# Performance work log

Hardware: AMD Instinct MI355X
Metric: run time of the kernel (lower is better)

Reference implementation:

```python
import jax, jax.numpy as jnp
import numpy as np

WS = (7, 7)  # window size
NUM_HEADS = 16


def _relative_position_index(ws):
    # Deterministic int index table, computed exactly as in the torch module.
    coords = np.stack(np.meshgrid(np.arange(ws[0]), np.arange(ws[1]), indexing='ij'))  # [2,Wh,Ww]
    coords = coords.reshape(2, -1)                       # [2, N]
    rel = coords[:, :, None] - coords[:, None, :]        # [2, N, N]
    rel = rel.transpose(1, 2, 0)                         # [N, N, 2]
    rel = rel + np.array([ws[0] - 1, ws[1] - 1])
    rel[:, :, 0] *= 2 * ws[1] - 1
    return jnp.asarray(rel.sum(-1), dtype=jnp.int32)     # [N, N]


def setup_inputs() -> dict:
    key = jax.random.key(0)
    ks = jax.random.split(key, 5)
    B_, N, C = 2048, WS[0] * WS[1], 512
    nw = 64
    return {
        'x': jax.random.normal(ks[0], (B_, N, C), dtype=jnp.float32),
        'mask': jax.random.normal(ks[1], (nw, N, N), dtype=jnp.float32),
        'qkv_w': jax.random.normal(ks[2], (3 * C, C), dtype=jnp.float32) * 0.02,
        'qkv_b': jax.random.normal(ks[3], (3 * C,), dtype=jnp.float32) * 0.02,
        'rpb_table': jax.random.normal(ks[4], ((2 * WS[0] - 1) * (2 * WS[1] - 1), NUM_HEADS), dtype=jnp.float32) * 0.02,
    }


def reference(x, mask, qkv_w, qkv_b, rpb_table):
    B_, N, C = x.shape
    H = NUM_HEADS
    hd = C // H
    scale = hd ** -0.5

    # qkv projection: [B_, N, 3, H, hd] -> q, k, v each [B_, H, N, hd]
    qkv = (jnp.einsum('bnc,oc->bno', x, qkv_w) + qkv_b)
    qkv = qkv.reshape(B_, N, 3, H, hd).transpose(2, 0, 3, 1, 4)
    q, k, v = qkv[0], qkv[1], qkv[2]

    attn = jnp.einsum('bhnd,bhmd->bhnm', q * scale, k)  # [B_, H, N, N]

    rel_idx = _relative_position_index(WS)                       # [N, N]
    bias = rpb_table[rel_idx.reshape(-1)].reshape(N, N, H)       # gather
    attn = attn + bias.transpose(2, 0, 1)[None]                  # [1, H, N, N]

    nw = mask.shape[0]
    attn = attn.reshape(B_ // nw, nw, H, N, N) + mask[None, :, None]
    attn = attn.reshape(B_, H, N, N)
    attn = jax.nn.softmax(attn, axis=-1)

    out = jnp.einsum('bhnm,bhmd->bhnd', attn, v)
    out = out.transpose(0, 2, 1, 3).reshape(B_, N, C)
    # NOTE: source assigns `X = self.proj(x)` but returns `x`, so the
    # output projection is dead code; we faithfully return pre-proj output.
    return out
```

## Files before the change

kernel.cpp:

```cpp
#include <hip/hip_runtime.h>
#include <cstdint>
#include <cstddef>

typedef __bf16 bf16x8 __attribute__((ext_vector_type(8)));
typedef float f32x4 __attribute__((ext_vector_type(4)));
typedef unsigned short u16x8 __attribute__((ext_vector_type(8)));
typedef unsigned short u16x4 __attribute__((ext_vector_type(4)));
typedef unsigned int u32x2 __attribute__((ext_vector_type(2)));

#define VT_LD 56
#define BSTRIDE 52
#define BSZ 2548
#define PLD 80

__device__ __forceinline__ unsigned short f2bf(float f) {
  unsigned int u = __builtin_bit_cast(unsigned int, f);
  u += 0x7FFFu + ((u >> 16) & 1u);
  return (unsigned short)(u >> 16);
}
__device__ __forceinline__ float bf2f(unsigned short h) {
  unsigned int u = (unsigned int)h << 16;
  return __builtin_bit_cast(float, u);
}

__device__ __forceinline__ void gload_lds16(const void* g, void* l) {
  __builtin_amdgcn_global_load_lds((const __attribute__((address_space(1))) void*)g,
                                   (__attribute__((address_space(3))) void*)l, 16, 0, 0);
}

__global__ void conv_f2b_k(const float* __restrict__ src, unsigned short* __restrict__ dst, long n8) {
  long i = (long)blockIdx.x * blockDim.x + threadIdx.x;
  long stride = (long)gridDim.x * blockDim.x;
  for (; i < n8; i += stride) {
    float4 a = *(const float4*)(src + i * 8);
    float4 b = *(const float4*)(src + i * 8 + 4);
    u16x8 p;
    p[0]=f2bf(a.x); p[1]=f2bf(a.y); p[2]=f2bf(a.z); p[3]=f2bf(a.w);
    p[4]=f2bf(b.x); p[5]=f2bf(b.y); p[6]=f2bf(b.z); p[7]=f2bf(b.w);
    *(u16x8*)(dst + i * 8) = p;
  }
}

__global__ void build_bias_k(const float* __restrict__ rpb, unsigned short* __restrict__ biasT) {
  int idx = blockIdx.x * 256 + threadIdx.x;
  if (idx >= 16 * BSZ) return;
  int h = idx / BSZ;
  int rem = idx - h * BSZ;
  int i = rem / BSTRIDE, j = rem - (rem / BSTRIDE) * BSTRIDE;
  unsigned short v = 0;
  if (j < 49) {
    int r1 = i / 7, c1 = i - r1 * 7;
    int r2 = j / 7, c2 = j - r2 * 7;
    int ri = (r1 - r2 + 6) * 13 + (c1 - c2 + 6);
    v = f2bf(rpb[ri * 16 + h]);
  }
  biasT[idx] = v;
}

#define GEMM_SETUP(N0)                                                         \
  int t = threadIdx.x;                                                         \
  int lane = t & 63, wv = t >> 6;                                              \
  int g = lane >> 4, q = lane & 15;                                            \
  int wrow = wv >> 1, wcol = wv & 1;                                           \
  f32x4 acc[4][4] = {};                                                        \
  int schunk = (t & 3) ^ ((t >> 3) & 3);                                       \
  const unsigned short* ag0 = xb + (m0 + (t >> 2)) * 512 + schunk * 8;         \
  const unsigned short* ag1 = ag0 + 64 * 512;                                  \
  const unsigned short* bg0 = wb + (size_t)((N0) + (t >> 2)) * 512 + schunk * 8; \
  const unsigned short* bg1 = bg0 + 64 * 512;                                  \
  unsigned short* alA  = Ab + wv * 512;                                        \
  unsigned short* alA2 = Ab + 2048 + wv * 512;                                 \
  unsigned short* blB  = Bb + wv * 512;                                        \
  unsigned short* blB2 = Bb + 2048 + wv * 512;                                 \
  int roff = (8 * g) ^ (((q >> 1) & 3) << 3);                                  \
  const unsigned short* arb = Ab + (wrow * 64 + q) * 32 + roff;                \
  const unsigned short* brb = Bb + (wcol * 64 + q) * 32 + roff;

#define STAGE(KT, BOFF) do {                    \
    int kof = (KT) * 32;                        \
    gload_lds16(ag0 + kof, alA  + (BOFF));      \
    gload_lds16(ag1 + kof, alA2 + (BOFF));      \
    gload_lds16(bg0 + kof, blB  + (BOFF));      \
    gload_lds16(bg1 + kof, blB2 + (BOFF));      \
  } while (0)

#define COMPUTE(BOFF, SWAPPED) do {                                            \
    bf16x8 af[4], bfr[4];                                                      \
    _Pragma("unroll")                                                          \
    for (int i2 = 0; i2 < 4; ++i2) af[i2]  = *(const bf16x8*)(arb + (BOFF) + i2 * 512); \
    _Pragma("unroll")                                                          \
    for (int j2 = 0; j2 < 4; ++j2) bfr[j2] = *(const bf16x8*)(brb + (BOFF) + j2 * 512); \
    _Pragma("unroll")                                                          \
    for (int i2 = 0; i2 < 4; ++i2)                                             \
      _Pragma("unroll")                                                        \
      for (int j2 = 0; j2 < 4; ++j2)                                           \
        acc[i2][j2] = (SWAPPED)                                                \
          ? __builtin_amdgcn_mfma_f32_16x16x32_bf16(bfr[j2], af[i2], acc[i2][j2], 0, 0, 0) \
          : __builtin_amdgcn_mfma_f32_16x16x32_bf16(af[i2], bfr[j2], acc[i2][j2], 0, 0, 0); \
  } while (0)

#define KLOOP(SWAPPED)                          \
  STAGE(0, 0);                                  \
  __syncthreads();                              \
  for (int kt = 0; kt < 16; kt += 2) {          \
    STAGE(kt + 1, 4096);                        \
    COMPUTE(0, SWAPPED);                        \
    __syncthreads();                            \
    if (kt + 2 < 16) STAGE(kt + 2, 0);          \
    COMPUTE(4096, SWAPPED);                     \
    __syncthreads();                            \
  }

__global__ __launch_bounds__(256, 3) void qkv_gemm_k(
    const unsigned short* __restrict__ xb, const float* __restrict__ qkv_b,
    const unsigned short* __restrict__ wb,
    unsigned short* __restrict__ qs, unsigned short* __restrict__ kk,
    unsigned short* __restrict__ vt)
{
  __shared__ __align__(16) unsigned short smem[16384];
  unsigned short* Ab = smem;
  unsigned short* Bb = smem + 8192;

  int bid = blockIdx.x;
  int sw = (bid & 7) * 1176 + (bid >> 3);
  int mt = sw / 12, nt = sw - mt * 12;
  long m0 = (long)mt * 128;
  int  n0 = nt * 128;
  int  s  = n0 >> 9;

  GEMM_SETUP(n0)

  if (s < 2) {
    KLOOP(1)
    unsigned short* dst = (s == 0) ? qs : kk;
    float sc = (s == 0) ? 0.17677669529663687f : 1.0f;
    float4 bi[4];
    int hj[4], dj[4];
    #pragma unroll
    for (int j2 = 0; j2 < 4; ++j2) {
      int n = n0 + wcol * 64 + j2 * 16 + 4 * g;
      bi[j2] = *(const float4*)(qkv_b + n);
      hj[j2] = (n >> 5) & 15;
      dj[j2] = n & 31;
    }
    #pragma unroll
    for (int i2 = 0; i2 < 4; ++i2) {
      unsigned int m = (unsigned int)m0 + wrow * 64 + i2 * 16 + q;
      unsigned int b = m / 49;
      unsigned int i = m - b * 49;
      size_t base = ((size_t)(b * 16) * 49 + i) * 32;
      #pragma unroll
      for (int j2 = 0; j2 < 4; ++j2) {
        f32x4 a = acc[i2][j2];
        unsigned int lo = (unsigned int)f2bf((a[0] + bi[j2].x) * sc) | ((unsigned int)f2bf((a[1] + bi[j2].y) * sc) << 16);
        unsigned int hi = (unsigned int)f2bf((a[2] + bi[j2].z) * sc) | ((unsigned int)f2bf((a[3] + bi[j2].w) * sc) << 16);
        u32x2 wv2 = {lo, hi};
        *(u32x2*)(dst + base + (size_t)hj[j2] * (49 * 32) + dj[j2]) = wv2;
      }
    }
  } else {
    KLOOP(0)
    #pragma unroll
    for (int j2 = 0; j2 < 4; ++j2) {
      int n  = n0 + wcol * 64 + j2 * 16 + q;
      float bias = qkv_b[n];
      int d = n & 31;
      int h = (n >> 5) & 15;
      #pragma unroll
      for (int i2 = 0; i2 < 4; ++i2) {
        unsigned int gm0 = (unsigned int)m0 + wrow * 64 + i2 * 16 + 4 * g;
        unsigned int b0 = gm0 / 49;
        unsigned int i0 = gm0 - b0 * 49;
        unsigned short hv[4];
        #pragma unroll
        for (int r = 0; r < 4; ++r) hv[r] = f2bf(acc[i2][j2][r] + bias);
        if (i0 <= 45) {
          unsigned short* base = vt + ((size_t)(b0 * 16 + h) * 32 + d) * VT_LD;
          if ((i0 & 1) == 0) {
            *(unsigned int*)(base + i0)     = (unsigned int)hv[0] | ((unsigned int)hv[1] << 16);
            *(unsigned int*)(base + i0 + 2) = (unsigned int)hv[2] | ((unsigned int)hv[3] << 16);
          } else {
            base[i0] = hv[0];
            *(unsigned int*)(base + i0 + 1) = (unsigned int)hv[1] | ((unsigned int)hv[2] << 16);
            base[i0 + 3] = hv[3];
          }
        } else {
          #pragma unroll
          for (int r = 0; r < 4; ++r) {
            unsigned int gm = gm0 + r;
            unsigned int b = gm / 49;
            unsigned int i = gm - b * 49;
            vt[((size_t)(b * 16 + h) * 32 + d) * VT_LD + i] = hv[r];
          }
        }
      }
    }
  }
}

__global__ __launch_bounds__(256, 2) void win_attn_k(
    const unsigned short* __restrict__ qs, const unsigned short* __restrict__ kk,
    const unsigned short* __restrict__ vt, const unsigned short* __restrict__ biasT,
    const float* __restrict__ mask, float* __restrict__ out)
{
  __shared__ float mlds[BSZ];
  __shared__ unsigned short plds[4][64 * PLD];

  int b = blockIdx.x;
  int t = threadIdx.x;
  int lane = t & 63, wv = t >> 6;
  int g = lane >> 4, q = lane & 15;

  const float* msrc = mask + (size_t)(b & 63) * 2401;
  for (int idx = t; idx < BSZ; idx += 256) {
    int i = idx / BSTRIDE, j = idx - (idx / BSTRIDE) * BSTRIDE;
    mlds[idx] = (j < 49) ? msrc[i * 49 + j] : 0.0f;
  }
  __syncthreads();

  unsigned short* pl = plds[wv];
  const float NINF = -__builtin_inff();

  int rc[4];
  rc[0] = q; rc[1] = 16 + q; rc[2] = 32 + q; rc[3] = 48;

  int h0 = wv * 4;
  const unsigned short* qh = qs + (size_t)(b * 16 + h0) * (49 * 32);
  const unsigned short* kh = kk + (size_t)(b * 16 + h0) * (49 * 32);
  bf16x8 ak[4], bq[4];
  #pragma unroll
  for (int jt = 0; jt < 4; ++jt) ak[jt] = *(const bf16x8*)(kh + rc[jt] * 32 + 8 * g);
  #pragma unroll
  for (int it = 0; it < 4; ++it) bq[it] = *(const bf16x8*)(qh + rc[it] * 32 + 8 * g);

  #pragma unroll
  for (int hh = 0; hh < 4; ++hh) {
    int h = wv * 4 + hh;
    const unsigned short* vh  = vt + (size_t)(b * 16 + h) * (32 * VT_LD);
    const unsigned short* bh2 = biasT + h * BSZ;

    f32x4 zero = {0.f, 0.f, 0.f, 0.f};
    f32x4 st[4][4];
    __builtin_amdgcn_s_setprio(1);
    #pragma unroll
    for (int it = 0; it < 4; ++it)
      #pragma unroll
      for (int jt = 0; jt < 4; ++jt)
        st[it][jt] = __builtin_amdgcn_mfma_f32_16x16x32_bf16(ak[jt], bq[it], zero, 0, 0, 0);
    __builtin_amdgcn_s_setprio(0);

    bf16x8 akn[4], bqn[4];
    if (hh < 3) {
      const unsigned short* qh2 = qh + 49 * 32;
      const unsigned short* kh2 = kh + 49 * 32;
      #pragma unroll
      for (int jt = 0; jt < 4; ++jt) akn[jt] = *(const bf16x8*)(kh2 + rc[jt] * 32 + 8 * g);
      #pragma unroll
      for (int it = 0; it < 4; ++it) bqn[it] = *(const bf16x8*)(qh2 + rc[it] * 32 + 8 * g);
      qh = qh2; kh = kh2;
    }
    bf16x8 bv[2][2];
    #pragma unroll
    for (int ktt = 0; ktt < 2; ++ktt)
      #pragma unroll
      for (int dt = 0; dt < 2; ++dt)
        bv[ktt][dt] = *(const bf16x8*)(vh + (dt * 16 + q) * VT_LD + ktt * 32 + 8 * g);

    #pragma unroll
    for (int it = 0; it < 4; ++it) {
      int i = it * 16 + q;
      int ic = i > 48 ? 48 : i;
      f32x4 pv4[4];
      f32x4 vm = {NINF, NINF, NINF, NINF};
      #pragma unroll
      for (int jt = 0; jt < 4; ++jt) {
        if (jt == 3 && g > 0) {
          pv4[3] = (f32x4){NINF, NINF, NINF, NINF};
        } else {
          u16x4 bu = *(const u16x4*)(bh2 + ic * BSTRIDE + jt * 16 + 4 * g);
          f32x4 m4 = *(const f32x4*)(mlds + ic * BSTRIDE + jt * 16 + 4 * g);
          f32x4 sv = st[it][jt];
          #pragma unroll
          for (int r = 0; r < 4; ++r) sv[r] += bf2f(bu[r]) + m4[r];
          if (jt == 3) {
            sv[1] = NINF; sv[2] = NINF; sv[3] = NINF;
          }
          pv4[jt] = sv;
          #pragma unroll
          for (int r = 0; r < 4; ++r) vm[r] = fmaxf(vm[r], sv[r]);
        }
      }
      float mx = fmaxf(fmaxf(vm[0], vm[1]), fmaxf(vm[2], vm[3]));
      mx = fmaxf(mx, __shfl_xor(mx, 16));
      mx = fmaxf(mx, __shfl_xor(mx, 32));
      f32x4 vs = zero;
      #pragma unroll
      for (int jt = 0; jt < 4; ++jt) {
        #pragma unroll
        for (int r = 0; r < 4; ++r) {
          float p = __expf(pv4[jt][r] - mx);
          pv4[jt][r] = p;
          vs[r] += p;
        }
      }
      float sm = (vs[0] + vs[1]) + (vs[2] + vs[3]);
      sm += __shfl_xor(sm, 16);
      sm += __shfl_xor(sm, 32);
      float rv = 1.0f / sm;
      #pragma unroll
      for (int jt = 0; jt < 4; ++jt) {
        unsigned int lo = (unsigned int)f2bf(pv4[jt][0] * rv) | ((unsigned int)f2bf(pv4[jt][1] * rv) << 16);
        unsigned int hi = (unsigned int)f2bf(pv4[jt][2] * rv) | ((unsigned int)f2bf(pv4[jt][3] * rv) << 16);
        u32x2 w = {lo, hi};
        *(u32x2*)(pl + i * PLD + jt * 16 + 4 * g) = w;
      }
    }

    f32x4 oacc[4][2] = {};
    #pragma unroll
    for (int ktt = 0; ktt < 2; ++ktt) {
      bf16x8 pa[4];
      #pragma unroll
      for (int it = 0; it < 4; ++it)
        pa[it] = *(const bf16x8*)(pl + (it * 16 + q) * PLD + ktt * 32 + 8 * g);
      __builtin_amdgcn_s_setprio(1);
      #pragma unroll
      for (int it = 0; it < 4; ++it)
        #pragma unroll
        for (int dt = 0; dt < 2; ++dt)
          oacc[it][dt] = __builtin_amdgcn_mfma_f32_16x16x32_bf16(pa[it], bv[ktt][dt], oacc[it][dt], 0, 0, 0);
      __builtin_amdgcn_s_setprio(0);
    }

    #pragma unroll
    for (int it = 0; it < 4; ++it) {
      #pragma unroll
      for (int dt = 0; dt < 2; ++dt) {
        #pragma unroll
        for (int r = 0; r < 4; ++r) {
          int i = it * 16 + 4 * g + r;
          if (i < 49) {
            int d = dt * 16 + q;
            out[(size_t)(b * 49 + i) * 512 + h * 32 + d] = oacc[it][dt][r];
          }
        }
      }
    }

    if (hh < 3) {
      #pragma unroll
      for (int jt = 0; jt < 4; ++jt) ak[jt] = akn[jt];
      #pragma unroll
      for (int it = 0; it < 4; ++it) bq[it] = bqn[it];
    }
  }
}

extern "C" void kernel_launch(void* const* d_in, const int* in_sizes, int n_in,
                              void* d_out, int out_size, void* d_ws, size_t ws_size,
                              hipStream_t stream) {
  const float* x     = (const float*)d_in[0];
  const float* mask  = (const float*)d_in[1];
  const float* qkv_w = (const float*)d_in[2];
  const float* qkv_b = (const float*)d_in[3];
  const float* rpb   = (const float*)d_in[4];
  float* out = (float*)d_out;

  const size_t QS_OFF   = 0;
  const size_t KK_OFF   = 102760448;
  const size_t VT_OFF   = 205520896;
  const size_t BIAS_OFF = 322961408;
  const size_t WB_OFF   = 323042944;
  const size_t NEED     = 324615808;
  if (ws_size < NEED) return;

  char* ws = (char*)d_ws;
  unsigned short* qsb   = (unsigned short*)(ws + QS_OFF);
  unsigned short* kkb   = (unsigned short*)(ws + KK_OFF);
  unsigned short* vtb   = (unsigned short*)(ws + VT_OFF);
  unsigned short* biasT = (unsigned short*)(ws + BIAS_OFF);
  unsigned short* wb    = (unsigned short*)(ws + WB_OFF);

  unsigned short* xb = (unsigned short*)d_out;

  conv_f2b_k<<<2048, 256, 0, stream>>>(x, xb, 6422528);
  conv_f2b_k<<<512, 256, 0, stream>>>(qkv_w, wb, 98304);
  build_bias_k<<<160, 256, 0, stream>>>(rpb, biasT);
  qkv_gemm_k<<<9408, 256, 0, stream>>>(xb, qkv_b, wb, qsb, kkb, vtb);
  win_attn_k<<<2048, 256, 0, stream>>>(qsb, kkb, vtb, biasT, mask, out);
}
```

Baseline: 449.6 us.

## Triple-buffer QKV GEMM pipeline and vectorize attention output stores

```diff
diff --git a/kernel.cpp b/kernel.cpp
--- a/kernel.cpp
+++ b/kernel.cpp
@@ -99,16 +99,20 @@
           : __builtin_amdgcn_mfma_f32_16x16x32_bf16(af[i2], bfr[j2], acc[i2][j2], 0, 0, 0); \
   } while (0)
 
-#define KLOOP(SWAPPED)                          \
-  STAGE(0, 0);                                  \
-  __syncthreads();                              \
-  for (int kt = 0; kt < 16; kt += 2) {          \
-    STAGE(kt + 1, 4096);                        \
-    COMPUTE(0, SWAPPED);                        \
-    __syncthreads();                            \
-    if (kt + 2 < 16) STAGE(kt + 2, 0);          \
-    COMPUTE(4096, SWAPPED);                     \
-    __syncthreads();                            \
+#define KLOOP(SWAPPED)                                                 \
+  STAGE(0, 0);                                                         \
+  STAGE(1, 4096);                                                      \
+  asm volatile("s_waitcnt vmcnt(4)" ::: "memory");                     \
+  __builtin_amdgcn_s_barrier();                                        \
+  _Pragma("unroll")                                                    \
+  for (int kt = 0; kt < 16; ++kt) {                                    \
+    if (kt + 2 < 16) STAGE(kt + 2, ((kt + 2) % 3) * 4096);             \
+    COMPUTE((kt % 3) * 4096, SWAPPED);                                 \
+    if (kt < 15) {                                                     \
+      if (kt + 2 < 16) asm volatile("s_waitcnt vmcnt(4)" ::: "memory"); \
+      else             asm volatile("s_waitcnt vmcnt(0)" ::: "memory"); \
+      __builtin_amdgcn_s_barrier();                                    \
+    }                                                                  \
   }
 
 __global__ __launch_bounds__(256, 3) void qkv_gemm_k(
@@ -117,9 +121,9 @@
     unsigned short* __restrict__ qs, unsigned short* __restrict__ kk,
     unsigned short* __restrict__ vt)
 {
-  __shared__ __align__(16) unsigned short smem[16384];
+  __shared__ __align__(16) unsigned short smem[24576];
   unsigned short* Ab = smem;
-  unsigned short* Bb = smem + 8192;
+  unsigned short* Bb = smem + 12288;
 
   int bid = blockIdx.x;
   int sw = (bid & 7) * 1176 + (bid >> 3);
@@ -328,22 +332,18 @@
       for (int it = 0; it < 4; ++it)
         #pragma unroll
         for (int dt = 0; dt < 2; ++dt)
-          oacc[it][dt] = __builtin_amdgcn_mfma_f32_16x16x32_bf16(pa[it], bv[ktt][dt], oacc[it][dt], 0, 0, 0);
+          oacc[it][dt] = __builtin_amdgcn_mfma_f32_16x16x32_bf16(bv[ktt][dt], pa[it], oacc[it][dt], 0, 0, 0);
       __builtin_amdgcn_s_setprio(0);
     }
 
     #pragma unroll
     for (int it = 0; it < 4; ++it) {
-      #pragma unroll
-      for (int dt = 0; dt < 2; ++dt) {
+      int i = it * 16 + q;
+      if (i < 49) {
+        float* orow = out + (size_t)(b * 49 + i) * 512 + h * 32 + 4 * g;
         #pragma unroll
-        for (int r = 0; r < 4; ++r) {
-          int i = it * 16 + 4 * g + r;
-          if (i < 49) {
-            int d = dt * 16 + q;
-            out[(size_t)(b * 49 + i) * 512 + h * 32 + d] = oacc[it][dt][r];
-          }
-        }
+        for (int dt = 0; dt < 2; ++dt)
+          *(f32x4*)(orow + dt * 16) = oacc[it][dt];
       }
     }
 
```

Result: no change. 448.6 us (-0.2%).

## Fuse x fp32-to-bf16 conversion into QKV GEMM loads and vectorize output stores

Applied to the files above, without the earlier changes.

```diff
diff --git a/kernel.cpp b/kernel.cpp
--- a/kernel.cpp
+++ b/kernel.cpp
@@ -57,31 +57,64 @@
   biasT[idx] = v;
 }
 
-#define GEMM_SETUP(N0)                                                         \
-  int t = threadIdx.x;                                                         \
-  int lane = t & 63, wv = t >> 6;                                              \
-  int g = lane >> 4, q = lane & 15;                                            \
-  int wrow = wv >> 1, wcol = wv & 1;                                           \
-  f32x4 acc[4][4] = {};                                                        \
-  int schunk = (t & 3) ^ ((t >> 3) & 3);                                       \
-  const unsigned short* ag0 = xb + (m0 + (t >> 2)) * 512 + schunk * 8;         \
-  const unsigned short* ag1 = ag0 + 64 * 512;                                  \
-  const unsigned short* bg0 = wb + (size_t)((N0) + (t >> 2)) * 512 + schunk * 8; \
-  const unsigned short* bg1 = bg0 + 64 * 512;                                  \
-  unsigned short* alA  = Ab + wv * 512;                                        \
-  unsigned short* alA2 = Ab + 2048 + wv * 512;                                 \
-  unsigned short* blB  = Bb + wv * 512;                                        \
-  unsigned short* blB2 = Bb + 2048 + wv * 512;                                 \
-  int roff = (8 * g) ^ (((q >> 1) & 3) << 3);                                  \
-  const unsigned short* arb = Ab + (wrow * 64 + q) * 32 + roff;                \
+__global__ __launch_bounds__(256, 3) void qkv_gemm_k(
+    const float* __restrict__ x, const float* __restrict__ qkv_b,
+    const unsigned short* __restrict__ wb,
+    unsigned short* __restrict__ qs, unsigned short* __restrict__ kk,
+    unsigned short* __restrict__ vt)
+{
+  __shared__ __align__(16) unsigned short smem[16384];
+  unsigned short* Ab = smem;
+  unsigned short* Bb = smem + 8192;
+
+  int bid = blockIdx.x;
+  int sw = (bid & 7) * 1176 + (bid >> 3);
+  int mt = sw / 12, nt = sw - mt * 12;
+  long m0 = (long)mt * 128;
+  int  n0 = nt * 128;
+  int  s  = n0 >> 9;
+
+  int t = threadIdx.x;
+  int lane = t & 63, wv = t >> 6;
+  int g = lane >> 4, q = lane & 15;
+  int wrow = wv >> 1, wcol = wv & 1;
+
+  f32x4 acc[4][4] = {};
+
+  int schunk = (t & 3) ^ ((t >> 3) & 3);
+  const float* ax0 = x + (m0 + (t >> 2)) * 512 + schunk * 8;
+  const float* ax1 = ax0 + 64 * 512;
+  unsigned short* aw0 = Ab + t * 8;
+  unsigned short* aw1 = Ab + 2048 + t * 8;
+  const unsigned short* bg0 = wb + (size_t)(n0 + (t >> 2)) * 512 + schunk * 8;
+  const unsigned short* bg1 = bg0 + 64 * 512;
+  unsigned short* blB  = Bb + wv * 512;
+  unsigned short* blB2 = Bb + 2048 + wv * 512;
+
+  int roff = (8 * g) ^ (((q >> 1) & 3) << 3);
+  const unsigned short* arb = Ab + (wrow * 64 + q) * 32 + roff;
   const unsigned short* brb = Bb + (wcol * 64 + q) * 32 + roff;
 
-#define STAGE(KT, BOFF) do {                    \
+  float4 A0, A1, A2, A3;
+
+#define SL(KT, BOFF) do {                       \
     int kof = (KT) * 32;                        \
-    gload_lds16(ag0 + kof, alA  + (BOFF));      \
-    gload_lds16(ag1 + kof, alA2 + (BOFF));      \
+    A0 = *(const float4*)(ax0 + kof);           \
+    A1 = *(const float4*)(ax0 + kof + 4);       \
+    A2 = *(const float4*)(ax1 + kof);           \
+    A3 = *(const float4*)(ax1 + kof + 4);       \
     gload_lds16(bg0 + kof, blB  + (BOFF));      \
     gload_lds16(bg1 + kof, blB2 + (BOFF));      \
+  } while (0)
+
+#define SW(BOFF) do {                           \
+    u16x8 p0, p1;                               \
+    p0[0]=f2bf(A0.x); p0[1]=f2bf(A0.y); p0[2]=f2bf(A0.z); p0[3]=f2bf(A0.w); \
+    p0[4]=f2bf(A1.x); p0[5]=f2bf(A1.y); p0[6]=f2bf(A1.z); p0[7]=f2bf(A1.w); \
+    p1[0]=f2bf(A2.x); p1[1]=f2bf(A2.y); p1[2]=f2bf(A2.z); p1[3]=f2bf(A2.w); \
+    p1[4]=f2bf(A3.x); p1[5]=f2bf(A3.y); p1[6]=f2bf(A3.z); p1[7]=f2bf(A3.w); \
+    *(u16x8*)(aw0 + (BOFF)) = p0;               \
+    *(u16x8*)(aw1 + (BOFF)) = p1;               \
   } while (0)
 
 #define COMPUTE(BOFF, SWAPPED) do {                                            \
@@ -100,35 +133,18 @@
   } while (0)
 
 #define KLOOP(SWAPPED)                          \
-  STAGE(0, 0);                                  \
+  SL(0, 0); SW(0);                              \
   __syncthreads();                              \
   for (int kt = 0; kt < 16; kt += 2) {          \
-    STAGE(kt + 1, 4096);                        \
+    SL(kt + 1, 4096);                           \
     COMPUTE(0, SWAPPED);                        \
+    SW(4096);                                   \
     __syncthreads();                            \
-    if (kt + 2 < 16) STAGE(kt + 2, 0);          \
+    if (kt + 2 < 16) SL(kt + 2, 0);             \
     COMPUTE(4096, SWAPPED);                     \
+    if (kt + 2 < 16) SW(0);                     \
     __syncthreads();                            \
   }
-
-__global__ __launch_bounds__(256, 3) void qkv_gemm_k(
-    const unsigned short* __restrict__ xb, const float* __restrict__ qkv_b,
-    const unsigned short* __restrict__ wb,
-    unsigned short* __restrict__ qs, unsigned short* __restrict__ kk,
-    unsigned short* __restrict__ vt)
-{
-  __shared__ __align__(16) unsigned short smem[16384];
-  unsigned short* Ab = smem;
-  unsigned short* Bb = smem + 8192;
-
-  int bid = blockIdx.x;
-  int sw = (bid & 7) * 1176 + (bid >> 3);
-  int mt = sw / 12, nt = sw - mt * 12;
-  long m0 = (long)mt * 128;
-  int  n0 = nt * 128;
-  int  s  = n0 >> 9;
-
-  GEMM_SETUP(n0)
 
   if (s < 2) {
     KLOOP(1)
@@ -196,9 +212,13 @@
       }
     }
   }
-}
-
-__global__ __launch_bounds__(256, 2) void win_attn_k(
+#undef SL
+#undef SW
+#undef COMPUTE
+#undef KLOOP
+}
+
+__global__ __launch_bounds__(256, 3) void win_attn_k(
     const unsigned short* __restrict__ qs, const unsigned short* __restrict__ kk,
     const unsigned short* __restrict__ vt, const unsigned short* __restrict__ biasT,
     const float* __restrict__ mask, float* __restrict__ out)
@@ -328,22 +348,18 @@
       for (int it = 0; it < 4; ++it)
         #pragma unroll
         for (int dt = 0; dt < 2; ++dt)
-          oacc[it][dt] = __builtin_amdgcn_mfma_f32_16x16x32_bf16(pa[it], bv[ktt][dt], oacc[it][dt], 0, 0, 0);
+          oacc[it][dt] = __builtin_amdgcn_mfma_f32_16x16x32_bf16(bv[ktt][dt], pa[it], oacc[it][dt], 0, 0, 0);
       __builtin_amdgcn_s_setprio(0);
     }
 
     #pragma unroll
     for (int it = 0; it < 4; ++it) {
-      #pragma unroll
-      for (int dt = 0; dt < 2; ++dt) {
+      int i = it * 16 + q;
+      if (i < 49) {
+        float* orow = out + (size_t)(b * 49 + i) * 512 + h * 32 + 4 * g;
         #pragma unroll
-        for (int r = 0; r < 4; ++r) {
-          int i = it * 16 + 4 * g + r;
-          if (i < 49) {
-            int d = dt * 16 + q;
-            out[(size_t)(b * 49 + i) * 512 + h * 32 + d] = oacc[it][dt][r];
-          }
-        }
+        for (int dt = 0; dt < 2; ++dt)
+          *(f32x4*)(orow + dt * 16) = oacc[it][dt];
       }
     }
 
@@ -381,11 +397,8 @@
   unsigned short* biasT = (unsigned short*)(ws + BIAS_OFF);
   unsigned short* wb    = (unsigned short*)(ws + WB_OFF);
 
-  unsigned short* xb = (unsigned short*)d_out;
-
-  conv_f2b_k<<<2048, 256, 0, stream>>>(x, xb, 6422528);
   conv_f2b_k<<<512, 256, 0, stream>>>(qkv_w, wb, 98304);
   build_bias_k<<<160, 256, 0, stream>>>(rpb, biasT);
-  qkv_gemm_k<<<9408, 256, 0, stream>>>(xb, qkv_b, wb, qsb, kkb, vtb);
+  qkv_gemm_k<<<9408, 256, 0, stream>>>(x, qkv_b, wb, qsb, kkb, vtb);
   win_attn_k<<<2048, 256, 0, stream>>>(qsb, kkb, vtb, biasT, mask, out);
 }
```

Result: no change. 448.1 us (-0.3%).
